# Performance work log

Hardware: AMD Instinct MI355X
Metric: run time of the kernel (lower is better)

## Reference

```python
import jax, jax.numpy as jnp
import numpy as np

R = 4          # args.search_range
D = 2 * R + 1  # window size per axis -> D*D = 81 output channels


def setup_inputs() -> dict:
    key = jax.random.key(0)
    k1, k2 = jax.random.split(key)
    B, C, H, W = 4, 128, 64, 128
    src = jax.random.normal(k1, (B, C, H, W), dtype=jnp.float32)
    tgt = jax.random.normal(k2, (B, C, H, W), dtype=jnp.float32)
    return {"src": src, "tgt": tgt}


def reference(src, tgt):
    # Faithful to the torch code: tgt is zero-padded by R on each spatial side,
    # then for output pixel (i, j) the window indices into the PADDED tensor are
    # I in [i-R, i+R], J in [j-R, j+R]. For i < R the index is negative, which in
    # torch wraps around -> reproduce with modular indexing.
    B, C, H, W = src.shape
    tp = jnp.pad(tgt, ((0, 0), (0, 0), (R, R), (R, R)))  # [B,C,H+2R,W+2R]
    Hp, Wp = H + 2 * R, W + 2 * R
    # col_idx[dj, j] = (j - R + dj) mod Wp
    col_idx = (jnp.arange(W)[None, :] - R + jnp.arange(D)[:, None]) % Wp  # [D,W]
    outs = []
    for di in range(D):  # small fixed loop over 9 row offsets
        row_idx = (jnp.arange(H) - R + di) % Hp        # [H]
        t_rows = tp[:, :, row_idx, :]                  # [B,C,H,Wp]
        t_win = t_rows[:, :, :, col_idx]               # [B,C,H,D,W]
        # channel-dot-product per pixel and per column offset
        outs.append(jnp.einsum('bchdw,bchw->bdhw', t_win, src))
    # channel ordering k = di*D + dj matches the original double loop over (I, J)
    return jnp.concatenate(outs, axis=1)  # [B, D*D, H, W]
```

## Files before the change

### kernel.cpp

```cpp
#include <hip/hip_runtime.h>
#include <stdint.h>

#define NB 4
#define NC 128
#define NH 64
#define NW 128
#define HW (NH * NW)
#define ND 9
#define NOUT (ND * ND)
#define CPW 32

__global__ __launch_bounds__(256, 4) void costvol_kernel(const float* __restrict__ src,
                                                         const float* __restrict__ tgt,
                                                         float* __restrict__ out) {
  const int tid  = threadIdx.x;
  const int lane = tid & 63;
  const int wave = tid >> 6;
  const int slice = blockIdx.x >> 5;
  const int di = slice % ND;
  const int b  = slice / ND;
  const int hp = blockIdx.x & 31;
  const int h  = (hp << 1) + (lane >> 5);
  const int w0 = (lane & 31) << 2;
  const int y  = h + di - 8;

  float acc[ND][4];
#pragma unroll
  for (int dj = 0; dj < ND; ++dj)
#pragma unroll
    for (int k = 0; k < 4; ++k) acc[dj][k] = 0.0f;

  const bool q0 = w0 >= 8;
  const bool q1 = w0 >= 4;

  if (y >= 0) {
    const float* spc = src + (size_t)((b * NC + wave * CPW) * NH + h) * NW + w0;
    const float* tpc = tgt + (size_t)((b * NC + wave * CPW) * NH + y) * NW;

#pragma unroll 4
    for (int c = 0; c < CPW; ++c) {
      const float4 sv = *(const float4*)spc;

      float t[12];
      {
        float4 t0, t1, t2;
        if (q0) t0 = *(const float4*)(tpc + w0 - 8);
        else    t0 = make_float4(0.f, 0.f, 0.f, 0.f);
        if (q1) t1 = *(const float4*)(tpc + w0 - 4);
        else    t1 = make_float4(0.f, 0.f, 0.f, 0.f);
        t2 = *(const float4*)(tpc + w0);
        t[0] = t0.x; t[1] = t0.y; t[2]  = t0.z; t[3]  = t0.w;
        t[4] = t1.x; t[5] = t1.y; t[6]  = t1.z; t[7]  = t1.w;
        t[8] = t2.x; t[9] = t2.y; t[10] = t2.z; t[11] = t2.w;
      }

#pragma unroll
      for (int dj = 0; dj < ND; ++dj) {
        acc[dj][0] = fmaf(sv.x, t[dj + 0], acc[dj][0]);
        acc[dj][1] = fmaf(sv.y, t[dj + 1], acc[dj][1]);
        acc[dj][2] = fmaf(sv.z, t[dj + 2], acc[dj][2]);
        acc[dj][3] = fmaf(sv.w, t[dj + 3], acc[dj][3]);
      }

      spc += HW;
      tpc += HW;
    }
  }

  __shared__ float lds[4][ND][64][4];
#pragma unroll
  for (int dj = 0; dj < ND; ++dj) {
    float4 v;
    v.x = acc[dj][0]; v.y = acc[dj][1]; v.z = acc[dj][2]; v.w = acc[dj][3];
    *(float4*)&lds[wave][dj][lane][0] = v;
  }
  __syncthreads();

  for (int s = tid; s < ND * 64; s += 256) {
    const int dj = s >> 6;
    const int l  = s & 63;
    const float4 r0 = *(const float4*)&lds[0][dj][l][0];
    const float4 r1 = *(const float4*)&lds[1][dj][l][0];
    const float4 r2 = *(const float4*)&lds[2][dj][l][0];
    const float4 r3 = *(const float4*)&lds[3][dj][l][0];
    float4 o;
    o.x = (r0.x + r1.x) + (r2.x + r3.x);
    o.y = (r0.y + r1.y) + (r2.y + r3.y);
    o.z = (r0.z + r1.z) + (r2.z + r3.z);
    o.w = (r0.w + r1.w) + (r2.w + r3.w);
    const int hh = (hp << 1) + (l >> 5);
    const int ww = (l & 31) << 2;
    *(float4*)(out + (size_t)(((b * NOUT + di * ND + dj) * NH + hh) * NW + ww)) = o;
  }
}

extern "C" void kernel_launch(void* const* d_in, const int* in_sizes, int n_in,
                              void* d_out, int out_size, void* d_ws, size_t ws_size,
                              hipStream_t stream) {
  const float* src = (const float*)d_in[0];
  const float* tgt = (const float*)d_in[1];
  float* out = (float*)d_out;
  costvol_kernel<<<dim3(NB * ND * 32), dim3(256), 0, stream>>>(src, tgt, out);
}
```

Baseline: 92.64 us.

## Rewrite cost volume as bf16 MFMA banded matmul with double-buffered LDS rows

Replaces the per-thread FP32 FMA correlation with a kernel where each block owns one output row. It converts src and tgt rows to bf16 in LDS and computes the 16x16 diagonal and sub-diagonal tiles of the src·tgt channel product using MFMA 16x16x32 instructions. The next tgt row is prefetched into a second LDS buffer while the current one is consumed. Results are scattered through LDS to form the 9 column offsets per row. This uses matrix cores and reuses the src row across all 9 row offsets, at the cost of bf16 precision loss and extra block-wide synchronisation per offset.

```diff
diff --git a/kernel.cpp b/kernel.cpp
--- a/kernel.cpp
+++ b/kernel.cpp
@@ -8,89 +8,149 @@
 #define HW (NH * NW)
 #define ND 9
 #define NOUT (ND * ND)
-#define CPW 32
+#define PROW 1040
 
-__global__ __launch_bounds__(256, 4) void costvol_kernel(const float* __restrict__ src,
+typedef __attribute__((ext_vector_type(8))) short short8;
+typedef __attribute__((ext_vector_type(4))) float f32x4;
+
+__device__ __forceinline__ ushort f2bf(float f) {
+  uint u = __float_as_uint(f);
+  u += 0x7FFFu + ((u >> 16) & 1u);
+  return (ushort)(u >> 16);
+}
+
+__global__ __launch_bounds__(512, 2) void costvol_kernel(const float* __restrict__ src,
                                                          const float* __restrict__ tgt,
                                                          float* __restrict__ out) {
+  __shared__ ushort srcP[16 * PROW];
+  __shared__ ushort tgtP[2][16 * PROW];
+  __shared__ float  outlds[ND * NW];
+
   const int tid  = threadIdx.x;
   const int lane = tid & 63;
   const int wave = tid >> 6;
-  const int slice = blockIdx.x >> 5;
-  const int di = slice % ND;
-  const int b  = slice / ND;
-  const int hp = blockIdx.x & 31;
-  const int h  = (hp << 1) + (lane >> 5);
-  const int w0 = (lane & 31) << 2;
-  const int y  = h + di - 8;
+  const int col  = lane & 15;
+  const int g    = lane >> 4;
 
-  float acc[ND][4];
+  const int xcd = blockIdx.x & 7;
+  const int b   = xcd >> 1;
+  const int h   = ((xcd & 1) << 5) | (blockIdx.x >> 3);
+
+  const int sc = (tid >> 5) << 3;
+  const int sn = (tid & 31) << 2;
+
+  const float* sbase = src + (size_t)(b * NC) * HW;
+  const float* tbase = tgt + (size_t)(b * NC) * HW;
+
+  {
+    float4 v[8];
 #pragma unroll
-  for (int dj = 0; dj < ND; ++dj)
+    for (int j = 0; j < 8; ++j)
+      v[j] = *(const float4*)(sbase + (size_t)(sc + j) * HW + h * NW + sn);
 #pragma unroll
-    for (int k = 0; k < 4; ++k) acc[dj][k] = 0.0f;
+    for (int i = 0; i < 4; ++i) {
+      short8 e;
+#pragma unroll
+      for (int j = 0; j < 8; ++j) e[j] = (short)f2bf(((const float*)&v[j])[i]);
+      *(short8*)&srcP[(tid >> 5) * PROW + (sn + i) * 8] = e;
+    }
+  }
+  {
+    const int y0 = (h - 8 < 0) ? 0 : (h - 8);
+    float4 v[8];
+#pragma unroll
+    for (int j = 0; j < 8; ++j)
+      v[j] = *(const float4*)(tbase + (size_t)(sc + j) * HW + y0 * NW + sn);
+#pragma unroll
+    for (int i = 0; i < 4; ++i) {
+      short8 e;
+#pragma unroll
+      for (int j = 0; j < 8; ++j) e[j] = (short)f2bf(((const float*)&v[j])[i]);
+      *(short8*)&tgtP[0][(tid >> 5) * PROW + (sn + i) * 8] = e;
+    }
+  }
+  __syncthreads();
 
-  const bool q0 = w0 >= 8;
-  const bool q1 = w0 >= 4;
+  const int m0 = wave << 4;
+  short8 A[4];
+#pragma unroll
+  for (int kk = 0; kk < 4; ++kk)
+    A[kk] = *(const short8*)&srcP[(4 * kk + g) * PROW + (m0 + col) * 8];
 
-  if (y >= 0) {
-    const float* spc = src + (size_t)((b * NC + wave * CPW) * NH + h) * NW + w0;
-    const float* tpc = tgt + (size_t)((b * NC + wave * CPW) * NH + y) * NW;
+  for (int di = 0; di < ND; ++di) {
+    const int p = di & 1;
+    const int y = h + di - 8;
 
-#pragma unroll 4
-    for (int c = 0; c < CPW; ++c) {
-      const float4 sv = *(const float4*)spc;
+    float4 v[8];
+    const bool havenext = (di < 8);
+    if (havenext) {
+      const int yn = (y + 1 < 0) ? 0 : (y + 1);
+#pragma unroll
+      for (int j = 0; j < 8; ++j)
+        v[j] = *(const float4*)(tbase + (size_t)(sc + j) * HW + yn * NW + sn);
+    }
 
-      float t[12];
-      {
-        float4 t0, t1, t2;
-        if (q0) t0 = *(const float4*)(tpc + w0 - 8);
-        else    t0 = make_float4(0.f, 0.f, 0.f, 0.f);
-        if (q1) t1 = *(const float4*)(tpc + w0 - 4);
-        else    t1 = make_float4(0.f, 0.f, 0.f, 0.f);
-        t2 = *(const float4*)(tpc + w0);
-        t[0] = t0.x; t[1] = t0.y; t[2]  = t0.z; t[3]  = t0.w;
-        t[4] = t1.x; t[5] = t1.y; t[6]  = t1.z; t[7]  = t1.w;
-        t[8] = t2.x; t[9] = t2.y; t[10] = t2.z; t[11] = t2.w;
+    if (y >= 0) {
+      const ushort* tp = tgtP[p];
+      short8 BD[4], BS[4];
+#pragma unroll
+      for (int kk = 0; kk < 4; ++kk)
+        BD[kk] = *(const short8*)&tp[(4 * kk + g) * PROW + (m0 + col) * 8];
+      if (wave) {
+#pragma unroll
+        for (int kk = 0; kk < 4; ++kk)
+          BS[kk] = *(const short8*)&tp[(4 * kk + g) * PROW + (m0 - 16 + col) * 8];
+      }
+
+      f32x4 accD = {0.f, 0.f, 0.f, 0.f};
+      f32x4 accS = {0.f, 0.f, 0.f, 0.f};
+#pragma unroll
+      for (int kk = 0; kk < 4; ++kk)
+        accD = __builtin_amdgcn_mfma_f32_16x16x32_bf16(A[kk], BD[kk], accD, 0, 0, 0);
+      if (wave) {
+#pragma unroll
+        for (int kk = 0; kk < 4; ++kk)
+          accS = __builtin_amdgcn_mfma_f32_16x16x32_bf16(A[kk], BS[kk], accS, 0, 0, 0);
       }
 
 #pragma unroll
-      for (int dj = 0; dj < ND; ++dj) {
-        acc[dj][0] = fmaf(sv.x, t[dj + 0], acc[dj][0]);
-        acc[dj][1] = fmaf(sv.y, t[dj + 1], acc[dj][1]);
-        acc[dj][2] = fmaf(sv.z, t[dj + 2], acc[dj][2]);
-        acc[dj][3] = fmaf(sv.w, t[dj + 3], acc[dj][3]);
+      for (int q = 0; q < 4; ++q) {
+        const int row = 4 * g + q;
+        const int w   = m0 + row;
+        const int djd = col - row + 8;
+        if (djd >= 0 && djd <= 8)
+          outlds[djd * NW + ((w + 4 * djd) & 127)] = accD[q];
+        if (wave) {
+          const int djs = col - row - 8;
+          if (djs >= 0 && djs <= 8)
+            outlds[djs * NW + ((w + 4 * djs) & 127)] = accS[q];
+        }
       }
+    }
 
-      spc += HW;
-      tpc += HW;
+    if (havenext) {
+#pragma unroll
+      for (int i = 0; i < 4; ++i) {
+        short8 e;
+#pragma unroll
+        for (int j = 0; j < 8; ++j) e[j] = (short)f2bf(((const float*)&v[j])[i]);
+        *(short8*)&tgtP[p ^ 1][(tid >> 5) * PROW + (sn + i) * 8] = e;
+      }
     }
-  }
 
-  __shared__ float lds[4][ND][64][4];
+    __syncthreads();
+
+    if (tid < ND * 32) {
+      const int dj = tid >> 5;
+      const int w  = (tid & 31) << 2;
+      f32x4 o = *(const f32x4*)&outlds[dj * NW + ((w + 4 * dj) & 127)];
+      const bool vb = (y >= 0);
 #pragma unroll
-  for (int dj = 0; dj < ND; ++dj) {
-    float4 v;
-    v.x = acc[dj][0]; v.y = acc[dj][1]; v.z = acc[dj][2]; v.w = acc[dj][3];
-    *(float4*)&lds[wave][dj][lane][0] = v;
-  }
-  __syncthreads();
-
-  for (int s = tid; s < ND * 64; s += 256) {
-    const int dj = s >> 6;
-    const int l  = s & 63;
-    const float4 r0 = *(const float4*)&lds[0][dj][l][0];
-    const float4 r1 = *(const float4*)&lds[1][dj][l][0];
-    const float4 r2 = *(const float4*)&lds[2][dj][l][0];
-    const float4 r3 = *(const float4*)&lds[3][dj][l][0];
-    float4 o;
-    o.x = (r0.x + r1.x) + (r2.x + r3.x);
-    o.y = (r0.y + r1.y) + (r2.y + r3.y);
-    o.z = (r0.z + r1.z) + (r2.z + r3.z);
-    o.w = (r0.w + r1.w) + (r2.w + r3.w);
-    const int hh = (hp << 1) + (l >> 5);
-    const int ww = (l & 31) << 2;
-    *(float4*)(out + (size_t)(((b * NOUT + di * ND + dj) * NH + hh) * NW + ww)) = o;
+      for (int i = 0; i < 4; ++i)
+        if (!vb || (w + i + dj < 8)) o[i] = 0.f;
+      *(f32x4*)(out + ((size_t)((b * NOUT + di * ND + dj) * NH + h)) * NW + w) = o;
+    }
+    __syncthreads();
   }
 }
 
@@ -100,5 +160,5 @@
   const float* src = (const float*)d_in[0];
   const float* tgt = (const float*)d_in[1];
   float* out = (float*)d_out;
-  costvol_kernel<<<dim3(NB * ND * 32), dim3(256), 0, stream>>>(src, tgt, out);
+  costvol_kernel<<<dim3(NB * NH), dim3(512), 0, stream>>>(src, tgt, out);
 }
```

After: 87.32 us. 1.06x faster.

## Rewrite cost volume as bf16 MFMA matmuls with LDS-staged sliding target rows

Applied to the files above, without the earlier changes.

Replaces the scalar FP32 FMA kernel with a bf16 MFMA formulation. Source and target rows are converted to bf16 and staged into LDS, and the target rows are kept in a 9-row ring buffer so each one is loaded once and reused across output rows. Each wave computes one row offset as 16x16 tile products and extracts the diagonal bands into an LDS output tile before writing coalesced stores. The grid is remapped to 256 blocks of 576 threads with an XCD-aware block ordering. Dropping to bf16 inputs reduces precision and may exceed the tolerance.

```diff
diff --git a/kernel.cpp b/kernel.cpp
--- a/kernel.cpp
+++ b/kernel.cpp
@@ -8,89 +8,134 @@
 #define HW (NH * NW)
 #define ND 9
 #define NOUT (ND * ND)
-#define CPW 32
+#define SH 4
+#define QW 32
+#define TROW 392
+#define SROW 264
+#define OTILE (ND * 32)
 
-__global__ __launch_bounds__(256, 4) void costvol_kernel(const float* __restrict__ src,
+typedef __attribute__((ext_vector_type(8))) short short8;
+typedef __attribute__((ext_vector_type(4))) float f32x4;
+
+__device__ __forceinline__ ushort f2bf(float f) {
+  uint u = __float_as_uint(f);
+  u += 0x7FFFu + ((u >> 16) & 1u);
+  return (ushort)(u >> 16);
+}
+
+__global__ __launch_bounds__(576, 1) void costvol_kernel(const float* __restrict__ src,
                                                          const float* __restrict__ tgt,
                                                          float* __restrict__ out) {
+  __shared__ ushort tgtS[9][16 * TROW];
+  __shared__ ushort srcS[SH][16 * SROW];
+  __shared__ float  outlds[ND * OTILE];
+
   const int tid  = threadIdx.x;
   const int lane = tid & 63;
   const int wave = tid >> 6;
-  const int slice = blockIdx.x >> 5;
-  const int di = slice % ND;
-  const int b  = slice / ND;
-  const int hp = blockIdx.x & 31;
-  const int h  = (hp << 1) + (lane >> 5);
-  const int w0 = (lane & 31) << 2;
-  const int y  = h + di - 8;
+  const int col  = lane & 15;
+  const int g    = lane >> 4;
 
-  float acc[ND][4];
-#pragma unroll
-  for (int dj = 0; dj < ND; ++dj)
-#pragma unroll
-    for (int k = 0; k < 4; ++k) acc[dj][k] = 0.0f;
+  const int xcd   = blockIdx.x & 7;
+  const int r     = blockIdx.x >> 3;
+  const int combo = ((r >> 4) << 3) | xcd;
+  const int b     = combo >> 2;
+  const int q     = combo & 3;
+  const int h0    = (r & 15) << 2;
 
-  const bool q0 = w0 >= 8;
-  const bool q1 = w0 >= 4;
+  const float* sb = src + (size_t)(b * NC) * HW;
+  const float* tb = tgt + (size_t)(b * NC) * HW;
 
-  if (y >= 0) {
-    const float* spc = src + (size_t)((b * NC + wave * CPW) * NH + h) * NW + w0;
-    const float* tpc = tgt + (size_t)((b * NC + wave * CPW) * NH + y) * NW;
-
-#pragma unroll 4
-    for (int c = 0; c < CPW; ++c) {
-      const float4 sv = *(const float4*)spc;
-
-      float t[12];
-      {
-        float4 t0, t1, t2;
-        if (q0) t0 = *(const float4*)(tpc + w0 - 8);
-        else    t0 = make_float4(0.f, 0.f, 0.f, 0.f);
-        if (q1) t1 = *(const float4*)(tpc + w0 - 4);
-        else    t1 = make_float4(0.f, 0.f, 0.f, 0.f);
-        t2 = *(const float4*)(tpc + w0);
-        t[0] = t0.x; t[1] = t0.y; t[2]  = t0.z; t[3]  = t0.w;
-        t[4] = t1.x; t[5] = t1.y; t[6]  = t1.z; t[7]  = t1.w;
-        t[8] = t2.x; t[9] = t2.y; t[10] = t2.z; t[11] = t2.w;
-      }
+  auto stage_tgt = [&](int y) {
+    ushort* dstS = tgtS[y % 9];
+    const float* py = tb + (size_t)y * NW;
+    for (int cell = tid; cell < 12 * 128; cell += 576) {
+      const int fc = cell % 12;
+      const int c  = cell / 12;
+      const int g0 = q * QW - 16 + 4 * fc;
+      const float4 v = *(const float4*)(py + (size_t)c * HW + (g0 < 0 ? 0 : g0));
+      ushort* d = dstS + (c >> 3) * TROW + (4 * fc) * 8 + (c & 7);
+      d[0]  = f2bf(v.x);
+      d[8]  = f2bf(v.y);
+      d[16] = f2bf(v.z);
+      d[24] = f2bf(v.w);
+    }
+  };
+  auto stage_src = [&](int hh) {
+    ushort* dstS = srcS[hh];
+    const float* ph = sb + (size_t)(h0 + hh) * NW + q * QW;
+    for (int cell = tid; cell < 8 * 128; cell += 576) {
+      const int fc = cell % 8;
+      const int c  = cell / 8;
+      const float4 v = *(const float4*)(ph + (size_t)c * HW + 4 * fc);
+      ushort* d = dstS + (c >> 3) * SROW + (4 * fc) * 8 + (c & 7);
+      d[0]  = f2bf(v.x);
+      d[8]  = f2bf(v.y);
+      d[16] = f2bf(v.z);
+      d[24] = f2bf(v.w);
+    }
+  };
 
 #pragma unroll
-      for (int dj = 0; dj < ND; ++dj) {
-        acc[dj][0] = fmaf(sv.x, t[dj + 0], acc[dj][0]);
-        acc[dj][1] = fmaf(sv.y, t[dj + 1], acc[dj][1]);
-        acc[dj][2] = fmaf(sv.z, t[dj + 2], acc[dj][2]);
-        acc[dj][3] = fmaf(sv.w, t[dj + 3], acc[dj][3]);
-      }
-
-      spc += HW;
-      tpc += HW;
-    }
-  }
-
-  __shared__ float lds[4][ND][64][4];
-#pragma unroll
-  for (int dj = 0; dj < ND; ++dj) {
-    float4 v;
-    v.x = acc[dj][0]; v.y = acc[dj][1]; v.z = acc[dj][2]; v.w = acc[dj][3];
-    *(float4*)&lds[wave][dj][lane][0] = v;
-  }
+  for (int hh = 0; hh < SH; ++hh) stage_src(hh);
+  for (int y = h0 - 8; y <= h0; ++y)
+    if (y >= 0) stage_tgt(y);
   __syncthreads();
 
-  for (int s = tid; s < ND * 64; s += 256) {
-    const int dj = s >> 6;
-    const int l  = s & 63;
-    const float4 r0 = *(const float4*)&lds[0][dj][l][0];
-    const float4 r1 = *(const float4*)&lds[1][dj][l][0];
-    const float4 r2 = *(const float4*)&lds[2][dj][l][0];
-    const float4 r3 = *(const float4*)&lds[3][dj][l][0];
-    float4 o;
-    o.x = (r0.x + r1.x) + (r2.x + r3.x);
-    o.y = (r0.y + r1.y) + (r2.y + r3.y);
-    o.z = (r0.z + r1.z) + (r2.z + r3.z);
-    o.w = (r0.w + r1.w) + (r2.w + r3.w);
-    const int hh = (hp << 1) + (l >> 5);
-    const int ww = (l & 31) << 2;
-    *(float4*)(out + (size_t)(((b * NOUT + di * ND + dj) * NH + hh) * NW + ww)) = o;
+  for (int hh = 0; hh < SH; ++hh) {
+    const int h = h0 + hh;
+    const int y = h + wave - 8;
+    if (y >= 0) {
+      const ushort* Bp = tgtS[y % 9];
+      const ushort* Ap = srcS[hh];
+      f32x4 aD0 = {0.f,0.f,0.f,0.f}, aS0 = {0.f,0.f,0.f,0.f};
+      f32x4 aD1 = {0.f,0.f,0.f,0.f}, aS1 = {0.f,0.f,0.f,0.f};
+#pragma unroll
+      for (int kk = 0; kk < 4; ++kk) {
+        const int ro = 4 * kk + g;
+        const short8 A0 = *(const short8*)&Ap[ro * SROW + col * 8];
+        const short8 A1 = *(const short8*)&Ap[ro * SROW + (16 + col) * 8];
+        const short8 B0 = *(const short8*)&Bp[ro * TROW + col * 8];
+        const short8 B1 = *(const short8*)&Bp[ro * TROW + (16 + col) * 8];
+        const short8 B2 = *(const short8*)&Bp[ro * TROW + (32 + col) * 8];
+        aS0 = __builtin_amdgcn_mfma_f32_16x16x32_bf16(A0, B0, aS0, 0, 0, 0);
+        aD0 = __builtin_amdgcn_mfma_f32_16x16x32_bf16(A0, B1, aD0, 0, 0, 0);
+        aS1 = __builtin_amdgcn_mfma_f32_16x16x32_bf16(A1, B1, aS1, 0, 0, 0);
+        aD1 = __builtin_amdgcn_mfma_f32_16x16x32_bf16(A1, B2, aD1, 0, 0, 0);
+      }
+      float* ol = &outlds[wave * OTILE];
+#pragma unroll
+      for (int qr = 0; qr < 4; ++qr) {
+        const int row = 4 * g + qr;
+        const int djd = col - row + 8;
+        const int djs = col - row - 8;
+        if (djd >= 0 && djd <= 8) {
+          ol[djd * 32 + ((row + 4 * djd) & 31)]      = aD0[qr];
+          ol[djd * 32 + ((16 + row + 4 * djd) & 31)] = aD1[qr];
+        }
+        if (djs >= 0 && djs <= 8) {
+          ol[djs * 32 + ((row + 4 * djs) & 31)]      = aS0[qr];
+          ol[djs * 32 + ((16 + row + 4 * djs) & 31)] = aS1[qr];
+        }
+      }
+    }
+    __syncthreads();
+
+    for (int s = tid; s < ND * ND * 8; s += 576) {
+      const int di = s / 72;
+      const int rr = s % 72;
+      const int dj = rr >> 3;
+      const int w4 = (rr & 7) << 2;
+      f32x4 o = *(const f32x4*)&outlds[di * OTILE + dj * 32 + ((w4 + 4 * dj) & 31)];
+      const bool vb = (h + di - 8) >= 0;
+      const int wg = q * QW + w4;
+#pragma unroll
+      for (int i = 0; i < 4; ++i)
+        if (!vb || (wg + i + dj < 8)) o[i] = 0.f;
+      *(f32x4*)(out + ((size_t)((b * NOUT + di * ND + dj) * NH + h)) * NW + wg) = o;
+    }
+    if (hh < SH - 1) stage_tgt(h + 1);
+    __syncthreads();
   }
 }
 
@@ -100,5 +145,5 @@
   const float* src = (const float*)d_in[0];
   const float* tgt = (const float*)d_in[1];
   float* out = (float*)d_out;
-  costvol_kernel<<<dim3(NB * ND * 32), dim3(256), 0, stream>>>(src, tgt, out);
+  costvol_kernel<<<dim3(256), dim3(576), 0, stream>>>(src, tgt, out);
 }
```

New measurement: 92.99 us. About the same (+0.4%).
